# Performance work log

Hardware: AMD Instinct MI355X
Metric: run time of the kernel (lower is better)

## Reference

```python
import jax, jax.numpy as jnp
import numpy as np

N_NODES = 50000


def _gcn(x, row, col, w, b, n):
    # add self loops
    loops = jnp.arange(n, dtype=row.dtype)
    row = jnp.concatenate([row, loops])
    col = jnp.concatenate([col, loops])
    h = x @ w  # [N, out]
    deg = jax.ops.segment_sum(jnp.ones(col.shape, h.dtype), col, num_segments=n)
    dinv = jnp.where(deg > 0, deg ** -0.5, 0.0)
    norm = dinv[row] * dinv[col]  # [E+N]
    msg = norm[:, None] * h[row]
    out = jax.ops.segment_sum(msg, col, num_segments=n)
    return out + b


def _edgeconv(x, row, col, w1, b1, w2, b2, n):
    x_i = x[col]            # target features
    x_j = x[row]            # source features
    t = jnp.concatenate([x_i, x_j - x_i], axis=1)  # [E, 2*hidden]
    m = jax.nn.relu(t @ w1 + b1) @ w2 + b2          # [E, hidden]
    agg = jax.ops.segment_max(m, col, num_segments=n)
    # PyG fills empty segments with 0, segment_max fills with -inf
    return jnp.where(jnp.isfinite(agg), agg, 0.0)


def setup_inputs() -> dict:
    key = jax.random.key(0)
    ks = jax.random.split(key, 10)
    n, e = N_NODES, 800000
    cin, ch, cout = 32, 64, 16
    x = jax.random.normal(ks[0], (n, cin), dtype=jnp.float32)
    edge_index = jax.random.randint(ks[1], (2, e), 0, n, dtype=jnp.int64)

    def glorot(k, shape):
        lim = (6.0 / (shape[0] + shape[1])) ** 0.5
        return jax.random.uniform(k, shape, jnp.float32, -lim, lim)

    return {
        "x": x,
        "edge_index": edge_index,
        "gcn1_w": glorot(ks[2], (cin, ch)),
        "gcn1_b": jnp.zeros((ch,), jnp.float32),
        "edge_w1": glorot(ks[3], (2 * ch, ch)),
        "edge_b1": jnp.zeros((ch,), jnp.float32),
        "edge_w2": glorot(ks[4], (ch, ch)),
        "edge_b2": jnp.zeros((ch,), jnp.float32),
        "gcn2_w": glorot(ks[5], (ch, cout)),
        "gcn2_b": jnp.zeros((cout,), jnp.float32),
    }


def reference(x, edge_index, gcn1_w, gcn1_b, edge_w1, edge_b1, edge_w2, edge_b2, gcn2_w, gcn2_b):
    n = x.shape[0]
    row, col = edge_index[0], edge_index[1]
    h = jnp.tanh(_gcn(x, row, col, gcn1_w, gcn1_b, n))
    h = jax.nn.relu(_edgeconv(h, row, col, edge_w1, edge_b1, edge_w2, edge_b2, n))
    out = _gcn(h, row, col, gcn2_w, gcn2_b, n)
    return out
```

## Files before the change

### kernel.cpp

```cpp
#include <hip/hip_runtime.h>


typedef __attribute__((ext_vector_type(8))) short short8;
typedef __attribute__((ext_vector_type(4))) float f32x4;
typedef __attribute__((ext_vector_type(8))) _Float16 f16x8;
typedef __attribute__((ext_vector_type(4))) _Float16 f16x4;
typedef __attribute__((ext_vector_type(2))) _Float16 f16x2;

#define FILL_CH 4096

__device__ __forceinline__ unsigned short f2bf(float x) {
    unsigned int u = __float_as_uint(x);
    return (unsigned short)((u + 0x7FFFu + ((u >> 16) & 1u)) >> 16);
}
__device__ __forceinline__ float bf2f(unsigned short h) {
    return __uint_as_float(((unsigned int)h) << 16);
}
__device__ __forceinline__ void splitT(float u, short& hi, short& lo) {
    unsigned int ub = __float_as_uint(u);
    hi = (short)(ub >> 16);
    float r = u - __uint_as_float(ub & 0xFFFF0000u);
    lo = (short)(__float_as_uint(r) >> 16);
}
__device__ __forceinline__ f16x8 relu8(f16x8 v) {
    f16x8 z = {0, 0, 0, 0, 0, 0, 0, 0};
#if __has_builtin(__builtin_elementwise_max)
    return __builtin_elementwise_max(v, z);
#else
    f16x8 o;
#pragma unroll
    for (int j = 0; j < 8; ++j) o[j] = v[j] > (_Float16)0 ? v[j] : (_Float16)0;
    return o;
#endif
}

#define ROR_ADD(s, CTRL)                                                         \
    s += __int_as_float(__builtin_amdgcn_update_dpp(                             \
        0, __float_as_int(s), (CTRL), 0xf, 0xf, false))
#define ROR8_ADD(s) ROR_ADD(s, 0x128)

__global__ __launch_bounds__(256) void k_cast_count(
        const int* __restrict__ col, const float4* __restrict__ x4,
        f16x4* __restrict__ xh4, int* __restrict__ bcnt, int E, int m4, int nb) {
    __shared__ int cnt[512];
    int tid = threadIdx.x;
    for (int i = tid; i < nb; i += 256) cnt[i] = 0;
    __syncthreads();
    int e0 = blockIdx.x * FILL_CH;
#pragma unroll
    for (int i = 0; i < 16; ++i) {
        int e = e0 + tid + i * 256;
        if (e < E) atomicAdd(&cnt[col[e] >> 7], 1);
    }
    int nth = gridDim.x * 256;
    for (int idx = blockIdx.x * 256 + tid; idx < m4; idx += nth) {
        float4 v = x4[idx];
        f16x4 o;
        o[0] = (_Float16)v.x; o[1] = (_Float16)v.y;
        o[2] = (_Float16)v.z; o[3] = (_Float16)v.w;
        xh4[idx] = o;
    }
    __syncthreads();
    for (int i = tid; i < nb; i += 256)
        if (cnt[i]) atomicAdd(&bcnt[i], cnt[i]);
}

__global__ __launch_bounds__(512) void k_bucket_scan(
        const int* __restrict__ bcnt, int* __restrict__ bbase,
        int* __restrict__ bcur, int* __restrict__ ptr, int nb, int n, int E) {
    __shared__ int wt[8];
    int tid = threadIdx.x;
    int lane = tid & 63, w = tid >> 6;
    int v = (tid < nb) ? bcnt[tid] : 0;
    int s = v;
    for (int off = 1; off < 64; off <<= 1) {
        int t = __shfl_up(s, off, 64);
        if (lane >= off) s += t;
    }
    if (lane == 63) wt[w] = s;
    __syncthreads();
    int pre = 0;
    for (int i = 0; i < 8; ++i) if (i < w) pre += wt[i];
    int excl = pre + s - v;
    if (tid < nb) { bbase[tid] = excl; bcur[tid] = excl; }
    if (tid == nb) bbase[tid] = E;
    if (tid == 0) ptr[n] = E;
}

__global__ __launch_bounds__(256) void k_fill_a(const int* __restrict__ row,
                                                const int* __restrict__ col,
                                                int* __restrict__ bcur,
                                                int2* __restrict__ stage, int E, int nb) {
    __shared__ int cnt[512];
    __shared__ int base[512];
    int tid = threadIdx.x;
    int e0 = blockIdx.x * FILL_CH;
    for (int i = tid; i < nb; i += 256) cnt[i] = 0;
    __syncthreads();
    int r[16], c[16];
#pragma unroll
    for (int i = 0; i < 16; ++i) {
        int e = e0 + tid + i * 256;
        if (e < E) {
            r[i] = row[e]; c[i] = col[e];
            atomicAdd(&cnt[c[i] >> 7], 1);
        } else c[i] = -1;
    }
    __syncthreads();
    for (int i = tid; i < nb; i += 256)
        base[i] = cnt[i] ? atomicAdd(&bcur[i], cnt[i]) : 0;
    __syncthreads();
    for (int i = tid; i < nb; i += 256) cnt[i] = 0;
    __syncthreads();
#pragma unroll
    for (int i = 0; i < 16; ++i) {
        if (c[i] >= 0) {
            int b = c[i] >> 7;
            int lp = atomicAdd(&cnt[b], 1);
            stage[base[b] + lp] = make_int2(r[i], c[i]);
        }
    }
}

__global__ __launch_bounds__(256) void k_fill_b2(
        const int* __restrict__ bbase, const int* __restrict__ bcur_end,
        const int2* __restrict__ stage, int* __restrict__ ptr,
        float* __restrict__ dinv, int* __restrict__ csr, int n) {
    __shared__ int lcnt[128];
    __shared__ int lcur[128];
    __shared__ int wtotS;
    int b = blockIdx.x, tid = threadIdx.x;
    int c0 = b << 7;
    int start = bbase[b], end = bcur_end[b];
    if (tid < 128) lcnt[tid] = 0;
    __syncthreads();
    for (int p = start + tid; p < end; p += 256)
        atomicAdd(&lcnt[stage[p].y & 127], 1);
    __syncthreads();
    int lane = tid & 63, w = tid >> 6;
    int v = (tid < 128) ? lcnt[tid] : 0;
    int s = v;
    for (int off = 1; off < 64; off <<= 1) {
        int t = __shfl_up(s, off, 64);
        if (lane >= off) s += t;
    }
    if (tid == 63) wtotS = s;
    __syncthreads();
    int excl = s - v + ((w == 1) ? wtotS : 0);
    if (tid < 128) {
        int c = c0 + tid;
        int basep = start + excl;
        lcur[tid] = basep;
        if (c < n) {
            ptr[c] = basep;
            dinv[c] = rsqrtf((float)(v + 1));
        }
    }
    __syncthreads();
    for (int p = start + tid; p < end; p += 256) {
        int2 rc = stage[p];
        int pos = atomicAdd(&lcur[rc.y & 127], 1);
        csr[pos] = rc.x;
    }
}

__global__ __launch_bounds__(256) void k_gather32(
        const int* __restrict__ ptr, const int* __restrict__ csr_row,
        const float* __restrict__ x, const _Float16* __restrict__ xh,
        const float* __restrict__ dinv, float* __restrict__ agg, int n) {
    int wid = blockIdx.x * 4 + (threadIdx.x >> 6);
    if (wid >= n) return;
    int lane = threadIdx.x & 63;
    int f4 = lane & 7, slot = lane >> 3;
    int v = wid;
    int start = ptr[v], end = ptr[v + 1];
    const f16x4* xh4 = (const f16x4*)xh;
    float sx = 0.f, sy = 0.f, sz = 0.f, sw = 0.f;
    int p = start + slot;
    int r = (p < end) ? csr_row[p] : 0;
    while (p < end) {
        int rcur = r;
        int pn = p + 8;
        if (pn < end) r = csr_row[pn];
        float dr = dinv[rcur];
        f16x4 xv = xh4[(size_t)rcur * 8 + f4];
        sx = fmaf(dr, (float)xv[0], sx);
        sy = fmaf(dr, (float)xv[1], sy);
        sz = fmaf(dr, (float)xv[2], sz);
        sw = fmaf(dr, (float)xv[3], sw);
        p = pn;
    }
    ROR8_ADD(sx); ROR8_ADD(sy); ROR8_ADD(sz); ROR8_ADD(sw);
#pragma unroll
    for (int off = 16; off < 64; off <<= 1) {
        sx += __shfl_xor(sx, off); sy += __shfl_xor(sy, off);
        sz += __shfl_xor(sz, off); sw += __shfl_xor(sw, off);
    }
    if (slot == 0) {
        float dv = dinv[v], d2 = dv * dv;
        float4 xv = ((const float4*)x)[(size_t)v * 8 + f4];
        float4 o;
        o.x = dv * sx + d2 * xv.x;
        o.y = dv * sy + d2 * xv.y;
        o.z = dv * sz + d2 * xv.z;
        o.w = dv * sw + d2 * xv.w;
        ((float4*)agg)[(size_t)v * 8 + f4] = o;
    }
}

__global__ __launch_bounds__(256, 1) void k_h1tab(
        const float* __restrict__ agg, const float* __restrict__ gw,
        const float* __restrict__ gb, const float* __restrict__ w1,
        const float* __restrict__ b1,
        _Float16* __restrict__ atab, _Float16* __restrict__ btab, int ntiles) {
    __shared__ float tileS[4][16 * 66];
    int lane = threadIdx.x & 63;
    int wv = threadIdx.x >> 6;
    int n16 = lane & 15, q = lane >> 4;
    float* T = tileS[wv];

    short8 gh[4], gl[4];
    float gbias[4];
#pragma unroll
    for (int t = 0; t < 4; ++t) {
        gbias[t] = gb[t * 16 + n16];
        short8 hh, ll;
#pragma unroll
        for (int j = 0; j < 8; ++j) {
            float w = gw[(q * 8 + j) * 64 + t * 16 + n16];
            unsigned short wh = f2bf(w);
            hh[j] = (short)wh;
            ll[j] = (short)f2bf(w - bf2f(wh));
        }
        gh[t] = hh; gl[t] = ll;
    }
    short8 th[4][2], tl[4][2], uh[4][2], ul[4][2];
    float bias1[4];
#pragma unroll
    for (int t = 0; t < 4; ++t) {
        bias1[t] = b1[t * 16 + n16];
#pragma unroll
        for (int ck = 0; ck < 2; ++ck) {
            short8 h1v, l1v, h2v, l2v;
#pragma unroll
            for (int j = 0; j < 8; ++j) {
                int d = ck * 32 + q * 8 + j;
                float wbv = w1[(64 + d) * 64 + t * 16 + n16];
                float wtv = w1[d * 64 + t * 16 + n16] - wbv;
                unsigned short x1 = f2bf(wtv);
                h1v[j] = (short)x1; l1v[j] = (short)f2bf(wtv - bf2f(x1));
                unsigned short x2 = f2bf(wbv);
                h2v[j] = (short)x2; l2v[j] = (short)f2bf(wbv - bf2f(x2));
            }
            th[t][ck] = h1v; tl[t][ck] = l1v;
            uh[t][ck] = h2v; ul[t][ck] = l2v;
        }
    }

    int nwaves = gridDim.x * 4;
    int wid = blockIdx.x * 4 + wv;
    for (int tile = wid; tile < ntiles; tile += nwaves) {
        int v0 = tile * 16;
        const float4* a4 = (const float4*)(agg + (size_t)(v0 + n16) * 32);
        float4 A0 = a4[2 * q], A1 = a4[2 * q + 1];
        float a[8] = {A0.x, A0.y, A0.z, A0.w, A1.x, A1.y, A1.z, A1.w};
        short8 ah, al;
#pragma unroll
        for (int j = 0; j < 8; ++j) { short h, l; splitT(a[j], h, l); ah[j] = h; al[j] = l; }
#pragma unroll
        for (int t = 0; t < 4; ++t) {
            f32x4 acc = (f32x4){gbias[t], gbias[t], gbias[t], gbias[t]};
            acc = __builtin_amdgcn_mfma_f32_16x16x32_bf16(ah, gh[t], acc, 0, 0, 0);
            acc = __builtin_amdgcn_mfma_f32_16x16x32_bf16(al, gh[t], acc, 0, 0, 0);
            acc = __builtin_amdgcn_mfma_f32_16x16x32_bf16(ah, gl[t], acc, 0, 0, 0);
#pragma unroll
            for (int i = 0; i < 4; ++i)
                T[(q * 4 + i) * 66 + t * 16 + n16] = tanhf(acc[i]);
        }
        float b[16];
#pragma unroll
        for (int j = 0; j < 8; ++j) {
            b[j]     = T[n16 * 66 + q * 8 + j];
            b[8 + j] = T[n16 * 66 + 32 + q * 8 + j];
        }
        short8 ah0, ah1, al0, al1;
#pragma unroll
        for (int j = 0; j < 8; ++j) {
            short h, l;
            splitT(b[j], h, l);      ah0[j] = h; al0[j] = l;
            splitT(b[8 + j], h, l);  ah1[j] = h; al1[j] = l;
        }
#pragma unroll
        for (int t = 0; t < 4; ++t) {
            f32x4 aa = (f32x4){bias1[t], bias1[t], bias1[t], bias1[t]};
            aa = __builtin_amdgcn_mfma_f32_16x16x32_bf16(ah0, th[t][0], aa, 0, 0, 0);
            aa = __builtin_amdgcn_mfma_f32_16x16x32_bf16(ah1, th[t][1], aa, 0, 0, 0);
            aa = __builtin_amdgcn_mfma_f32_16x16x32_bf16(al0, th[t][0], aa, 0, 0, 0);
            aa = __builtin_amdgcn_mfma_f32_16x16x32_bf16(al1, th[t][1], aa, 0, 0, 0);
            aa = __builtin_amdgcn_mfma_f32_16x16x32_bf16(ah0, tl[t][0], aa, 0, 0, 0);
            aa = __builtin_amdgcn_mfma_f32_16x16x32_bf16(ah1, tl[t][1], aa, 0, 0, 0);
            f32x4 bb = (f32x4){0.f, 0.f, 0.f, 0.f};
            bb = __builtin_amdgcn_mfma_f32_16x16x32_bf16(ah0, uh[t][0], bb, 0, 0, 0);
            bb = __builtin_amdgcn_mfma_f32_16x16x32_bf16(ah1, uh[t][1], bb, 0, 0, 0);
            bb = __builtin_amdgcn_mfma_f32_16x16x32_bf16(al0, uh[t][0], bb, 0, 0, 0);
            bb = __builtin_amdgcn_mfma_f32_16x16x32_bf16(al1, uh[t][1], bb, 0, 0, 0);
            bb = __builtin_amdgcn_mfma_f32_16x16x32_bf16(ah0, ul[t][0], bb, 0, 0, 0);
            bb = __builtin_amdgcn_mfma_f32_16x16x32_bf16(ah1, ul[t][1], bb, 0, 0, 0);
#pragma unroll
            for (int i = 0; i < 4; ++i) {
                size_t off = (size_t)(v0 + q * 4 + i) * 64 + t * 16 + n16;
                atab[off] = (_Float16)aa[i];
                btab[off] = (_Float16)bb[i];
            }
        }
    }
}

__global__ __launch_bounds__(256) void k_edge_mlp(
        const int* __restrict__ ptr, const int* __restrict__ csr_row,
        const _Float16* __restrict__ atab, const _Float16* __restrict__ btab,
        const float* __restrict__ w2, const float* __restrict__ b2,
        const float* __restrict__ wg, _Float16* __restrict__ h2h, int n) {
    int lane = threadIdx.x & 63;
    int n16 = lane & 15, q = lane >> 4;

    f16x8 wh[4][2];
    float bias[4];
    float wgf[4][4];
#pragma unroll
    for (int t = 0; t < 4; ++t) {
        bias[t] = b2[t * 16 + n16];
#pragma unroll
        for (int jj = 0; jj < 4; ++jj)
            wgf[t][jj] = wg[(t * 16 + n16) * 16 + q * 4 + jj];
#pragma unroll
        for (int ck = 0; ck < 2; ++ck) {
            f16x8 hh;
#pragma unroll
            for (int j = 0; j < 8; ++j)
                hh[j] = (_Float16)w2[(ck * 32 + q * 8 + j) * 64 + t * 16 + n16];
            wh[t][ck] = hh;
        }
    }

    int nwaves = gridDim.x * 4;
    int wid = blockIdx.x * 4 + (threadIdx.x >> 6);

    for (int c = wid; c < n; c += nwaves) {
        int st = ptr[c], ed = ptr[c + 1];
        const f16x8* a8 = (const f16x8*)(atab + (size_t)c * 64);
        f16x8 A0 = a8[q], A1 = a8[4 + q];
        float red[4] = {0.f, 0.f, 0.f, 0.f};

        int p0 = st;
        int nfull = (ed - st) >> 4;
        for (int ft = 0; ft < nfull; ++ft, p0 += 16) {
            int r = csr_row[p0 + n16];
            const f16x8* b8 = (const f16x8*)(btab + (size_t)r * 64);
            f16x8 u0 = relu8(A0 + b8[q]);
            f16x8 u1 = relu8(A1 + b8[4 + q]);
#pragma unroll
            for (int t = 0; t < 4; ++t) {
                f32x4 acc = (f32x4){bias[t], bias[t], bias[t], bias[t]};
                acc = __builtin_amdgcn_mfma_f32_16x16x32_f16(u0, wh[t][0], acc, 0, 0, 0);
                acc = __builtin_amdgcn_mfma_f32_16x16x32_f16(u1, wh[t][1], acc, 0, 0, 0);
                red[t] = fmaxf(red[t], fmaxf(fmaxf(acc[0], acc[1]), fmaxf(acc[2], acc[3])));
            }
        }
        int rem = ed - p0;
        if (rem > 0) {
            f16x8 u0 = {0, 0, 0, 0, 0, 0, 0, 0};
            f16x8 u1 = {0, 0, 0, 0, 0, 0, 0, 0};
            if (n16 < rem) {
                int r = csr_row[p0 + n16];
                const f16x8* b8 = (const f16x8*)(btab + (size_t)r * 64);
                u0 = relu8(A0 + b8[q]);
                u1 = relu8(A1 + b8[4 + q]);
            }
#pragma unroll
            for (int t = 0; t < 4; ++t) {
                f32x4 acc = (f32x4){bias[t], bias[t], bias[t], bias[t]};
                acc = __builtin_amdgcn_mfma_f32_16x16x32_f16(u0, wh[t][0], acc, 0, 0, 0);
                acc = __builtin_amdgcn_mfma_f32_16x16x32_f16(u1, wh[t][1], acc, 0, 0, 0);
#pragma unroll
                for (int i = 0; i < 4; ++i)
                    if (q * 4 + i < rem) red[t] = fmaxf(red[t], acc[i]);
            }
        }
#pragma unroll
        for (int t = 0; t < 4; ++t) {
            red[t] = fmaxf(red[t], __shfl_xor(red[t], 16));
            red[t] = fmaxf(red[t], __shfl_xor(red[t], 32));
        }
        float part[4];
#pragma unroll
        for (int jj = 0; jj < 4; ++jj) {
            part[jj] = red[0] * wgf[0][jj];
            part[jj] = fmaf(red[1], wgf[1][jj], part[jj]);
            part[jj] = fmaf(red[2], wgf[2][jj], part[jj]);
            part[jj] = fmaf(red[3], wgf[3][jj], part[jj]);
            ROR_ADD(part[jj], 0x121);
            ROR_ADD(part[jj], 0x122);
            ROR_ADD(part[jj], 0x124);
            ROR_ADD(part[jj], 0x128);
        }
        if (n16 == 0) {
            f16x4 ph;
            ph[0] = (_Float16)part[0]; ph[1] = (_Float16)part[1];
            ph[2] = (_Float16)part[2]; ph[3] = (_Float16)part[3];
            ((f16x4*)(h2h + (size_t)c * 16))[q] = ph;
        }
    }
}

__global__ __launch_bounds__(256) void k_gcn2_gather(
        const int* __restrict__ ptr, const int* __restrict__ csr_row,
        const _Float16* __restrict__ h2h, const float* __restrict__ dinv,
        const float* __restrict__ bg, float* __restrict__ out, int n) {
    int wid = blockIdx.x * 4 + (threadIdx.x >> 6);
    if (wid >= n) return;
    int lane = threadIdx.x & 63;
    int f2 = lane & 7, slot = lane >> 3;
    int c = wid;
    int start = ptr[c], end = ptr[c + 1];
    const f16x2* h22 = (const f16x2*)h2h;
    float sx = 0.f, sy = 0.f;
    int p = start + slot;
    int r = (p < end) ? csr_row[p] : 0;
    while (p < end) {
        int rcur = r;
        int pn = p + 8;
        if (pn < end) r = csr_row[pn];
        float dr = dinv[rcur];
        f16x2 hv = h22[(size_t)rcur * 8 + f2];
        sx = fmaf(dr, (float)hv[0], sx);
        sy = fmaf(dr, (float)hv[1], sy);
        p = pn;
    }
    ROR8_ADD(sx); ROR8_ADD(sy);
#pragma unroll
    for (int off = 16; off < 64; off <<= 1) {
        sx += __shfl_xor(sx, off);
        sy += __shfl_xor(sy, off);
    }
    if (slot == 0) {
        float dv = dinv[c];
        f16x2 hv = h22[(size_t)c * 8 + f2];
        float2 o;
        o.x = bg[2 * f2]     + dv * (dv * (float)hv[0] + sx);
        o.y = bg[2 * f2 + 1] + dv * (dv * (float)hv[1] + sy);
        ((float2*)out)[(size_t)c * 8 + f2] = o;
    }
}

extern "C" void kernel_launch(void* const* d_in, const int* in_sizes, int n_in,
                              void* d_out, int out_size, void* d_ws, size_t ws_size,
                              hipStream_t stream) {
    const float* x   = (const float*)d_in[0];
    const int*   ei  = (const int*)d_in[1];
    const float* g1w = (const float*)d_in[2];
    const float* g1b = (const float*)d_in[3];
    const float* ew1 = (const float*)d_in[4];
    const float* eb1 = (const float*)d_in[5];
    const float* ew2 = (const float*)d_in[6];
    const float* eb2 = (const float*)d_in[7];
    const float* g2w = (const float*)d_in[8];
    const float* g2b = (const float*)d_in[9];
    float* out = (float*)d_out;
    float* ws  = (float*)d_ws;

    const int n = in_sizes[0] / 32;
    const int E = in_sizes[1] / 2;
    const int* row = ei;
    const int* col = ei + E;
    const int ntiles = (n + 15) / 16;
    const int nbuck = (n + 127) >> 7;

    size_t npad    = ((size_t)n + 63) & ~(size_t)63;
    size_t o_misc  = 0;
    size_t o_ptr   = npad;
    size_t o_csr   = o_ptr + npad + 64;
    size_t o_dinv  = o_csr + (size_t)E;
    size_t o_atab  = o_dinv + npad;
    size_t o_btab  = o_atab + (size_t)n * 32;
    size_t o_agg   = o_btab + (size_t)n * 32;
    size_t o_xh    = o_agg + (size_t)n * 32;
    size_t o_h2h   = o_xh + (size_t)n * 16;
    size_t o_stage = o_h2h + (size_t)n * 8;
    size_t o_bcur  = o_stage + (size_t)E * 2;

    int*      bcnt   = (int*)(ws + o_misc);
    int*      bbase  = (int*)(ws + o_misc) + 512;
    int*      ptr    = (int*)(ws + o_ptr);
    int*      csr    = (int*)(ws + o_csr);
    float*    dinv   = ws + o_dinv;
    _Float16* atab   = (_Float16*)(ws + o_atab);
    _Float16* btab   = (_Float16*)(ws + o_btab);
    float*    agg    = ws + o_agg;
    _Float16* xh     = (_Float16*)(ws + o_xh);
    _Float16* h2h    = (_Float16*)(ws + o_h2h);
    int2*     stage  = (int2*)(ws + o_stage);
    int*      bcur   = (int*)(ws + o_bcur);

    int nblk = (n + 3) / 4;
    int fill_nb = (E + FILL_CH - 1) / FILL_CH;
    int m4 = n * 8;

    hipMemsetAsync(bcnt, 0, 512 * sizeof(int), stream);
    k_cast_count<<<fill_nb, 256, 0, stream>>>(col, (const float4*)x, (f16x4*)xh,
                                              bcnt, E, m4, nbuck);
    k_bucket_scan<<<1, 512, 0, stream>>>(bcnt, bbase, bcur, ptr, nbuck, n, E);
    k_fill_a<<<fill_nb, 256, 0, stream>>>(row, col, bcur, stage, E, nbuck);
    k_fill_b2<<<nbuck, 256, 0, stream>>>(bbase, bcur, stage, ptr, dinv, csr, n);
    k_gather32<<<nblk, 256, 0, stream>>>(ptr, csr, x, xh, dinv, agg, n);
    k_h1tab<<<256, 256, 0, stream>>>(agg, g1w, g1b, ew1, eb1, atab, btab, ntiles);
    k_edge_mlp<<<2048, 256, 0, stream>>>(ptr, csr, atab, btab, ew2, eb2, g2w, h2h, n);
    k_gcn2_gather<<<nblk, 256, 0, stream>>>(ptr, csr, h2h, dinv, g2b, out, n);
}
```

Measured before the change: 200.9 us.

## Pack staging entries, drop memset via per-block counts, prefetch edge rows

Each count block now writes its bucket counts to its own slot, and the single-block scan sums those slots, so the memset and global atomics go away. Staging entries shrink from int2 to one int that packs the row with the low 7 bits of the column, halving staging traffic. The edge MLP loop prefetches the next tile's csr row indices, adds bias after the max instead of seeding the accumulator, and raises wave priority around the MFMA block. The risks are a serial scan over about 196 chunks in one block, and packing that assumes row indices fit in 24 bits.

New measurement: 223.7 us. +11.3%, slower.

```diff
diff --git a/kernel.cpp b/kernel.cpp
--- a/kernel.cpp
+++ b/kernel.cpp
@@ -41,10 +41,10 @@
 
 __global__ __launch_bounds__(256) void k_cast_count(
         const int* __restrict__ col, const float4* __restrict__ x4,
-        f16x4* __restrict__ xh4, int* __restrict__ bcnt, int E, int m4, int nb) {
+        f16x4* __restrict__ xh4, int* __restrict__ pcnt, int E, int m4, int nb) {
     __shared__ int cnt[512];
     int tid = threadIdx.x;
-    for (int i = tid; i < nb; i += 256) cnt[i] = 0;
+    for (int i = tid; i < 512; i += 256) cnt[i] = 0;
     __syncthreads();
     int e0 = blockIdx.x * FILL_CH;
 #pragma unroll
@@ -61,17 +61,18 @@
         xh4[idx] = o;
     }
     __syncthreads();
-    for (int i = tid; i < nb; i += 256)
-        if (cnt[i]) atomicAdd(&bcnt[i], cnt[i]);
+    for (int i = tid; i < 512; i += 256)
+        pcnt[blockIdx.x * 512 + i] = cnt[i];
 }
 
 __global__ __launch_bounds__(512) void k_bucket_scan(
-        const int* __restrict__ bcnt, int* __restrict__ bbase,
+        const int* __restrict__ pcnt, int nchunks, int* __restrict__ bbase,
         int* __restrict__ bcur, int* __restrict__ ptr, int nb, int n, int E) {
     __shared__ int wt[8];
     int tid = threadIdx.x;
     int lane = tid & 63, w = tid >> 6;
-    int v = (tid < nb) ? bcnt[tid] : 0;
+    int v = 0;
+    for (int k = 0; k < nchunks; ++k) v += pcnt[k * 512 + tid];
     int s = v;
     for (int off = 1; off < 64; off <<= 1) {
         int t = __shfl_up(s, off, 64);
@@ -90,7 +91,7 @@
 __global__ __launch_bounds__(256) void k_fill_a(const int* __restrict__ row,
                                                 const int* __restrict__ col,
                                                 int* __restrict__ bcur,
-                                                int2* __restrict__ stage, int E, int nb) {
+                                                int* __restrict__ stage, int E, int nb) {
     __shared__ int cnt[512];
     __shared__ int base[512];
     int tid = threadIdx.x;
@@ -117,14 +118,14 @@
         if (c[i] >= 0) {
             int b = c[i] >> 7;
             int lp = atomicAdd(&cnt[b], 1);
-            stage[base[b] + lp] = make_int2(r[i], c[i]);
+            stage[base[b] + lp] = (r[i] << 7) | (c[i] & 127);
         }
     }
 }
 
 __global__ __launch_bounds__(256) void k_fill_b2(
         const int* __restrict__ bbase, const int* __restrict__ bcur_end,
-        const int2* __restrict__ stage, int* __restrict__ ptr,
+        const int* __restrict__ stage, int* __restrict__ ptr,
         float* __restrict__ dinv, int* __restrict__ csr, int n) {
     __shared__ int lcnt[128];
     __shared__ int lcur[128];
@@ -135,7 +136,7 @@
     if (tid < 128) lcnt[tid] = 0;
     __syncthreads();
     for (int p = start + tid; p < end; p += 256)
-        atomicAdd(&lcnt[stage[p].y & 127], 1);
+        atomicAdd(&lcnt[stage[p] & 127], 1);
     __syncthreads();
     int lane = tid & 63, w = tid >> 6;
     int v = (tid < 128) ? lcnt[tid] : 0;
@@ -158,9 +159,9 @@
     }
     __syncthreads();
     for (int p = start + tid; p < end; p += 256) {
-        int2 rc = stage[p];
-        int pos = atomicAdd(&lcur[rc.y & 127], 1);
-        csr[pos] = rc.x;
+        int vv = stage[p];
+        int pos = atomicAdd(&lcur[vv & 127], 1);
+        csr[pos] = vv >> 7;
     }
 }
 
@@ -342,6 +343,7 @@
             wh[t][ck] = hh;
         }
     }
+    const f32x4 z4 = (f32x4){0.f, 0.f, 0.f, 0.f};
 
     int nwaves = gridDim.x * 4;
     int wid = blockIdx.x * 4 + (threadIdx.x >> 6);
@@ -352,40 +354,47 @@
         f16x8 A0 = a8[q], A1 = a8[4 + q];
         float red[4] = {0.f, 0.f, 0.f, 0.f};
 
-        int p0 = st;
-        int nfull = (ed - st) >> 4;
-        for (int ft = 0; ft < nfull; ++ft, p0 += 16) {
-            int r = csr_row[p0 + n16];
-            const f16x8* b8 = (const f16x8*)(btab + (size_t)r * 64);
+        int deg = ed - st;
+        int nfull = deg >> 4;
+        int rem = deg & 15;
+        int remBase = st + (nfull << 4);
+        int rrem = (rem > 0 && n16 < rem) ? csr_row[remBase + n16] : 0;
+        int r = (nfull > 0) ? csr_row[st + n16] : 0;
+
+        for (int ft = 0; ft < nfull; ++ft) {
+            int rcur = r;
+            if (ft + 1 < nfull) r = csr_row[st + (ft + 1) * 16 + n16];
+            const f16x8* b8 = (const f16x8*)(btab + (size_t)rcur * 64);
             f16x8 u0 = relu8(A0 + b8[q]);
             f16x8 u1 = relu8(A1 + b8[4 + q]);
+            __builtin_amdgcn_s_setprio(1);
 #pragma unroll
             for (int t = 0; t < 4; ++t) {
-                f32x4 acc = (f32x4){bias[t], bias[t], bias[t], bias[t]};
-                acc = __builtin_amdgcn_mfma_f32_16x16x32_f16(u0, wh[t][0], acc, 0, 0, 0);
-                acc = __builtin_amdgcn_mfma_f32_16x16x32_f16(u1, wh[t][1], acc, 0, 0, 0);
-                red[t] = fmaxf(red[t], fmaxf(fmaxf(acc[0], acc[1]), fmaxf(acc[2], acc[3])));
+                f32x4 a = __builtin_amdgcn_mfma_f32_16x16x32_f16(u0, wh[t][0], z4, 0, 0, 0);
+                a = __builtin_amdgcn_mfma_f32_16x16x32_f16(u1, wh[t][1], a, 0, 0, 0);
+                float mx = fmaxf(fmaxf(a[0], a[1]), fmaxf(a[2], a[3]));
+                red[t] = fmaxf(red[t], mx + bias[t]);
             }
-        }
-        int rem = ed - p0;
+            __builtin_amdgcn_s_setprio(0);
+        }
         if (rem > 0) {
             f16x8 u0 = {0, 0, 0, 0, 0, 0, 0, 0};
             f16x8 u1 = {0, 0, 0, 0, 0, 0, 0, 0};
             if (n16 < rem) {
-                int r = csr_row[p0 + n16];
-                const f16x8* b8 = (const f16x8*)(btab + (size_t)r * 64);
+                const f16x8* b8 = (const f16x8*)(btab + (size_t)rrem * 64);
                 u0 = relu8(A0 + b8[q]);
                 u1 = relu8(A1 + b8[4 + q]);
             }
+            __builtin_amdgcn_s_setprio(1);
 #pragma unroll
             for (int t = 0; t < 4; ++t) {
-                f32x4 acc = (f32x4){bias[t], bias[t], bias[t], bias[t]};
-                acc = __builtin_amdgcn_mfma_f32_16x16x32_f16(u0, wh[t][0], acc, 0, 0, 0);
-                acc = __builtin_amdgcn_mfma_f32_16x16x32_f16(u1, wh[t][1], acc, 0, 0, 0);
+                f32x4 a = __builtin_amdgcn_mfma_f32_16x16x32_f16(u0, wh[t][0], z4, 0, 0, 0);
+                a = __builtin_amdgcn_mfma_f32_16x16x32_f16(u1, wh[t][1], a, 0, 0, 0);
 #pragma unroll
                 for (int i = 0; i < 4; ++i)
-                    if (q * 4 + i < rem) red[t] = fmaxf(red[t], acc[i]);
+                    if (q * 4 + i < rem) red[t] = fmaxf(red[t], a[i] + bias[t]);
             }
+            __builtin_amdgcn_s_setprio(0);
         }
 #pragma unroll
         for (int t = 0; t < 4; ++t) {
@@ -478,7 +487,7 @@
 
     size_t npad    = ((size_t)n + 63) & ~(size_t)63;
     size_t o_misc  = 0;
-    size_t o_ptr   = npad;
+    size_t o_ptr   = 1024;
     size_t o_csr   = o_ptr + npad + 64;
     size_t o_dinv  = o_csr + (size_t)E;
     size_t o_atab  = o_dinv + npad;
@@ -489,8 +498,7 @@
     size_t o_stage = o_h2h + (size_t)n * 8;
     size_t o_bcur  = o_stage + (size_t)E * 2;
 
-    int*      bcnt   = (int*)(ws + o_misc);
-    int*      bbase  = (int*)(ws + o_misc) + 512;
+    int*      bbase  = (int*)(ws + o_misc);
     int*      ptr    = (int*)(ws + o_ptr);
     int*      csr    = (int*)(ws + o_csr);
     float*    dinv   = ws + o_dinv;
@@ -499,17 +507,17 @@
     float*    agg    = ws + o_agg;
     _Float16* xh     = (_Float16*)(ws + o_xh);
     _Float16* h2h    = (_Float16*)(ws + o_h2h);
-    int2*     stage  = (int2*)(ws + o_stage);
+    int*      stage  = (int*)(ws + o_stage);
+    int*      pcnt   = (int*)(ws + o_stage);
     int*      bcur   = (int*)(ws + o_bcur);
 
     int nblk = (n + 3) / 4;
     int fill_nb = (E + FILL_CH - 1) / FILL_CH;
     int m4 = n * 8;
 
-    hipMemsetAsync(bcnt, 0, 512 * sizeof(int), stream);
     k_cast_count<<<fill_nb, 256, 0, stream>>>(col, (const float4*)x, (f16x4*)xh,
-                                              bcnt, E, m4, nbuck);
-    k_bucket_scan<<<1, 512, 0, stream>>>(bcnt, bbase, bcur, ptr, nbuck, n, E);
+                                              pcnt, E, m4, nbuck);
+    k_bucket_scan<<<1, 512, 0, stream>>>(pcnt, fill_nb, bbase, bcur, ptr, nbuck, n, E);
     k_fill_a<<<fill_nb, 256, 0, stream>>>(row, col, bcur, stage, E, nbuck);
     k_fill_b2<<<nbuck, 256, 0, stream>>>(bbase, bcur, stage, ptr, dinv, csr, n);
     k_gather32<<<nblk, 256, 0, stream>>>(ptr, csr, x, xh, dinv, agg, n);
```
